# Optimization experiments

Hardware: AMD Instinct MI355X
Metric: run time of the kernel (lower is better)

## Reference

```python
import jax, jax.numpy as jnp
import numpy as np

INPUT_DIM = 8
HIDDEN_DIM = 128
MID = 50
T = 4096
# original: tsteps = linspace(t0, t1, int(2 + (t1-t0)//0.1)); with t1-t0 == 1.0,
# 1.0//0.1 == 9.0 in float arithmetic -> 11 points -> 10 uniform Euler substeps.
K_SUB = 10


def setup_inputs() -> dict:
    key = jax.random.key(0)
    ks = jax.random.split(key, 12)
    x = jax.random.normal(ks[0], (T, INPUT_DIM), dtype=jnp.float32)
    # arange pairs (2i, 2i+1): every interval has t1 - t0 == 1.0
    dt = jnp.arange(T * 2, dtype=jnp.float32).reshape(T, 2)
    s = 0.1  # init.normal_(std=0.1) in LODEFunc; reuse for heads
    W1 = jax.random.normal(ks[1], (INPUT_DIM + HIDDEN_DIM, MID), dtype=jnp.float32) * s
    b1 = jnp.zeros((MID,), dtype=jnp.float32)
    W2 = jax.random.normal(ks[2], (MID, HIDDEN_DIM), dtype=jnp.float32) * s
    b2 = jnp.zeros((HIDDEN_DIM,), dtype=jnp.float32)
    Wls1 = jax.random.normal(ks[3], (HIDDEN_DIM, HIDDEN_DIM), dtype=jnp.float32) * s
    bls1 = jax.random.normal(ks[4], (HIDDEN_DIM,), dtype=jnp.float32) * s
    wls2 = jax.random.normal(ks[5], (HIDDEN_DIM,), dtype=jnp.float32) * s
    bls2 = jax.random.normal(ks[6], (), dtype=jnp.float32) * s
    Wlm1 = jax.random.normal(ks[7], (HIDDEN_DIM, HIDDEN_DIM), dtype=jnp.float32) * s
    blm1 = jax.random.normal(ks[8], (HIDDEN_DIM,), dtype=jnp.float32) * s
    return {"x": x, "dt": dt, "W1": W1, "b1": b1, "W2": W2, "b2": b2,
            "Wls1": Wls1, "bls1": bls1, "wls2": wls2, "bls2": bls2,
            "Wlm1": Wlm1, "blm1": blm1}


def reference(x, dt, W1, b1, W2, b2, Wls1, bls1, wls2, bls2, Wlm1, blm1):
    def ode_func(z, xi):
        # LODEFunc: tanh(Linear(tanh(Linear(cat(z, x)))))
        zx = jnp.concatenate([z, xi])  # [H + I]
        h1 = jnp.tanh(zx @ W1 + b1)    # [50]
        return jnp.tanh(h1 @ W2 + b2)  # [H]

    def step(z, inp):
        xi, dti = inp
        hstep = (dti[1] - dti[0]) / K_SUB  # uniform Euler step (0 interval -> no-op)
        z = jax.lax.fori_loop(0, K_SUB, lambda j, zz: zz + hstep * ode_func(zz, xi), z)
        pre_sigma = jnp.tanh(z @ Wls1 + bls1)
        sigma = jax.nn.softplus(pre_sigma @ wls2 + bls2)
        pre_mu = jnp.tanh(z @ Wlm1 + blm1)
        mu = pre_mu @ wls2 + bls2  # NOTE: original reuses self.ls2 for mu (faithful)
        return z, (mu, sigma)

    z0 = jnp.zeros((HIDDEN_DIM,), dtype=x.dtype)
    _, (mu_out, sigma_out) = jax.lax.scan(step, z0, (x, dt))
    return mu_out[:, None], sigma_out[:, None]  # each [T, 1]
```

## Files before the change

kernel.cpp:

```cpp
#include <hip/hip_runtime.h>
#include <hip/hip_bf16.h>

#define T_STEPS 4096
#define HID 128
#define INP 8
#define MID 50
#define KSUB 10

__device__ __forceinline__ float rlane(float v, int i){
    return __int_as_float(__builtin_amdgcn_readlane(__float_as_int(v), i));
}

__device__ __forceinline__ float fast_tanh(float x){
    float e = __expf(2.0f * x);
    return 1.0f - 2.0f / (e + 1.0f);
}
__device__ __forceinline__ float softplus_f(float x){
    return (x > 20.0f) ? x : __logf(1.0f + __expf(x));
}

__device__ __forceinline__ void wg_barrier(){
    asm volatile("s_waitcnt lgkmcnt(0)\n\ts_barrier" ::: "memory");
}

__global__ __launch_bounds__(384, 2)
void lode_kernel(const float* __restrict__ x, const float* __restrict__ dt,
                 const float* __restrict__ W1, const float* __restrict__ b1,
                 const float* __restrict__ W2, const float* __restrict__ b2,
                 const float* __restrict__ Wls1, const float* __restrict__ bls1,
                 const float* __restrict__ wls2, const float* __restrict__ bls2,
                 const float* __restrict__ Wlm1, const float* __restrict__ blm1,
                 float* __restrict__ out)
{
    __shared__ __align__(16) float pbuf[2][4][64];
    __shared__ __align__(16) float zsnap[2][HID];
    __shared__ __align__(16) float WhL[2][HID*HID];

    const int tid = threadIdx.x;
    const int wid = tid >> 6;
    const int l   = tid & 63;

    {
        float4*       d0 = reinterpret_cast<float4*>(&WhL[0][0]);
        const float4* s0 = reinterpret_cast<const float4*>(Wls1);
        for (int i = tid; i < HID*HID/4; i += 384) d0[i] = s0[i];
        float4*       d1 = reinterpret_cast<float4*>(&WhL[1][0]);
        const float4* s1 = reinterpret_cast<const float4*>(Wlm1);
        for (int i = tid; i < HID*HID/4; i += 384) d1[i] = s1[i];
    }
    wg_barrier();

    if (wid < 4){
        __builtin_amdgcn_s_setprio(1);
        const int base = wid << 5;
        const int lc   = (l < MID) ? l : 0;

        float w1h[32];
        #pragma unroll
        for (int i = 0; i < 32; ++i){
            const float v = W1[(base + i)*MID + lc];
            w1h[i] = (l < MID) ? v : 0.0f;
        }
        float w1x[INP];
        #pragma unroll
        for (int j = 0; j < INP; ++j){
            const float v = W1[(HID + j)*MID + lc];
            w1x[j] = (wid == 0 && l < MID) ? v : 0.0f;
        }
        const float b1c = (wid == 0 && l < MID) ? b1[lc] : 0.0f;

        const int jc = base + (l & 31);
        float w2c[MID];
        #pragma unroll
        for (int k = 0; k < MID; ++k) w2c[k] = W2[k*HID + jc];
        const float b2c = b2[jc];

        float zj = 0.0f;

        float4 xa  = *reinterpret_cast<const float4*>(&x[0]);
        float4 xb  = *reinterpret_cast<const float4*>(&x[4]);
        float2 dtc = *reinterpret_cast<const float2*>(&dt[0]);

        for (int t = 0; t < T_STEPS; ++t){
            const int tn = (t + 1 < T_STEPS) ? t + 1 : t;
            const float4 xan = *reinterpret_cast<const float4*>(&x[tn*INP]);
            const float4 xbn = *reinterpret_cast<const float4*>(&x[tn*INP + 4]);
            const float2 dtn = *reinterpret_cast<const float2*>(&dt[2*tn]);

            float xacc = b1c;
            xacc = fmaf(xa.x, w1x[0], xacc); xacc = fmaf(xa.y, w1x[1], xacc);
            xacc = fmaf(xa.z, w1x[2], xacc); xacc = fmaf(xa.w, w1x[3], xacc);
            xacc = fmaf(xb.x, w1x[4], xacc); xacc = fmaf(xb.y, w1x[5], xacc);
            xacc = fmaf(xb.z, w1x[6], xacc); xacc = fmaf(xb.w, w1x[7], xacc);
            const float hstep = (dtc.y - dtc.x) * (1.0f / KSUB);

            #pragma unroll 2
            for (int s = 0; s < KSUB; ++s){
                float a0 = xacc, a1 = 0.0f, a2 = 0.0f, a3 = 0.0f;
                #pragma unroll
                for (int i = 0; i < 32; i += 4){
                    a0 = fmaf(rlane(zj, i+0), w1h[i+0], a0);
                    a1 = fmaf(rlane(zj, i+1), w1h[i+1], a1);
                    a2 = fmaf(rlane(zj, i+2), w1h[i+2], a2);
                    a3 = fmaf(rlane(zj, i+3), w1h[i+3], a3);
                }
                pbuf[s & 1][wid][l] = (a0 + a1) + (a2 + a3);
                wg_barrier();

                const float p0 = pbuf[s & 1][0][l];
                const float p1 = pbuf[s & 1][1][l];
                const float p2 = pbuf[s & 1][2][l];
                const float p3 = pbuf[s & 1][3][l];
                const float h1v = fast_tanh((p0 + p1) + (p2 + p3));

                float d0 = 0.0f, d1 = 0.0f, d2 = 0.0f, d3 = 0.0f;
                #pragma unroll
                for (int k = 0; k < 48; k += 4){
                    d0 = fmaf(rlane(h1v, k+0), w2c[k+0], d0);
                    d1 = fmaf(rlane(h1v, k+1), w2c[k+1], d1);
                    d2 = fmaf(rlane(h1v, k+2), w2c[k+2], d2);
                    d3 = fmaf(rlane(h1v, k+3), w2c[k+3], d3);
                }
                d0 = fmaf(rlane(h1v, 48), w2c[48], d0);
                d1 = fmaf(rlane(h1v, 49), w2c[49], d1);
                const float d = (d0 + d1) + (d2 + d3);
                zj += hstep * fast_tanh(b2c + d);
            }

            if (l < 32) zsnap[t & 1][base + l] = zj;

            xa = xan; xb = xbn; dtc = dtn;
        }
        wg_barrier();
    } else {
        const float* __restrict__ Wh = (wid == 4) ? &WhL[0][0] : &WhL[1][0];
        const float* __restrict__ bh = (wid == 4) ? bls1 : blm1;
        float2 bhp;   bhp.x = bh[2*l];     bhp.y = bh[2*l+1];
        float2 wls2p; wls2p.x = wls2[2*l]; wls2p.y = wls2[2*l+1];
        const float bls2s = bls2[0];

        for (int t = 0; t <= T_STEPS; ++t){
            if (t < T_STEPS){
                #pragma unroll 2
                for (int s = 0; s < KSUB; ++s) wg_barrier();
            } else {
                wg_barrier();
            }
            if (t == 0) continue;
            const int ts = t - 1;
            const float* zs = &zsnap[ts & 1][0];
            float px = bhp.x, py = bhp.y;
            #pragma unroll 4
            for (int k = 0; k < HID; k += 4){
                const float4 zv = *reinterpret_cast<const float4*>(&zs[k]);
                const float2 a0 = *reinterpret_cast<const float2*>(&Wh[(k+0)*HID + 2*l]);
                const float2 a1 = *reinterpret_cast<const float2*>(&Wh[(k+1)*HID + 2*l]);
                const float2 a2 = *reinterpret_cast<const float2*>(&Wh[(k+2)*HID + 2*l]);
                const float2 a3 = *reinterpret_cast<const float2*>(&Wh[(k+3)*HID + 2*l]);
                px = fmaf(zv.x, a0.x, px); py = fmaf(zv.x, a0.y, py);
                px = fmaf(zv.y, a1.x, px); py = fmaf(zv.y, a1.y, py);
                px = fmaf(zv.z, a2.x, px); py = fmaf(zv.z, a2.y, py);
                px = fmaf(zv.w, a3.x, px); py = fmaf(zv.w, a3.y, py);
            }
            px = fast_tanh(px); py = fast_tanh(py);
            float r = px*wls2p.x + py*wls2p.y;
            #pragma unroll
            for (int off = 1; off < 64; off <<= 1) r += __shfl_xor(r, off, 64);
            if (l == 0){
                if (wid == 4) out[T_STEPS + ts] = softplus_f(r + bls2s);
                else          out[ts]           = r + bls2s;
            }
        }
    }
}

extern "C" void kernel_launch(void* const* d_in, const int* in_sizes, int n_in,
                              void* d_out, int out_size, void* d_ws, size_t ws_size,
                              hipStream_t stream)
{
    const float* x    = (const float*)d_in[0];
    const float* dt   = (const float*)d_in[1];
    const float* W1   = (const float*)d_in[2];
    const float* b1   = (const float*)d_in[3];
    const float* W2   = (const float*)d_in[4];
    const float* b2   = (const float*)d_in[5];
    const float* Wls1 = (const float*)d_in[6];
    const float* bls1 = (const float*)d_in[7];
    const float* wls2 = (const float*)d_in[8];
    const float* bls2 = (const float*)d_in[9];
    const float* Wlm1 = (const float*)d_in[10];
    const float* blm1 = (const float*)d_in[11];
    float* out = (float*)d_out;

    hipLaunchKernelGGL(lode_kernel, dim3(1), dim3(384), 0, stream,
                       x, dt, W1, b1, W2, b2, Wls1, bls1, wls2, bls2, Wlm1, blm1, out);
}
```

Before: 23.05 ms.

## Interleave head-wave matvec across substep barriers and use packed FMA

The two head waves now split their 128x128 matvec for the previous timestep into chunks done between the ten substep barriers, instead of waiting through all barriers and then doing the whole matvec in one go. The reduction and output write are spread over the last two slots, and the final timestep is handled after the loop. The accumulation also switches to a two-wide vector FMA so the compiler can emit packed FP32 FMAs. The aim is to keep the head waves from delaying the barrier-synchronised critical path of the ODE waves, at the cost of more complex control flow.

Result: faster. 18.48 ms, median of 2 (-19.8%).

```diff
diff --git a/kernel.cpp b/kernel.cpp
--- a/kernel.cpp
+++ b/kernel.cpp
@@ -6,6 +6,19 @@
 #define INP 8
 #define MID 50
 #define KSUB 10
+
+typedef float v2f __attribute__((ext_vector_type(2)));
+
+__device__ __forceinline__ v2f mk2(float a, float b){ v2f r; r.x = a; r.y = b; return r; }
+__device__ __forceinline__ v2f bc2(float s){ v2f r; r.x = s; r.y = s; return r; }
+
+__device__ __forceinline__ v2f fma2(v2f a, v2f b, v2f c){
+#if __has_builtin(__builtin_elementwise_fma)
+    return __builtin_elementwise_fma(a, b, c);
+#else
+    c.x = fmaf(a.x, b.x, c.x); c.y = fmaf(a.y, b.y, c.y); return c;
+#endif
+}
 
 __device__ __forceinline__ float rlane(float v, int i){
     return __int_as_float(__builtin_amdgcn_readlane(__float_as_int(v), i));
@@ -135,34 +148,67 @@
     } else {
         const float* __restrict__ Wh = (wid == 4) ? &WhL[0][0] : &WhL[1][0];
         const float* __restrict__ bh = (wid == 4) ? bls1 : blm1;
-        float2 bhp;   bhp.x = bh[2*l];     bhp.y = bh[2*l+1];
-        float2 wls2p; wls2p.x = wls2[2*l]; wls2p.y = wls2[2*l+1];
+        const v2f bhp   = mk2(bh[2*l], bh[2*l+1]);
+        const v2f wls2p = mk2(wls2[2*l], wls2[2*l+1]);
         const float bls2s = bls2[0];
 
-        for (int t = 0; t <= T_STEPS; ++t){
-            if (t < T_STEPS){
-                #pragma unroll 2
-                for (int s = 0; s < KSUB; ++s) wg_barrier();
-            } else {
+        for (int t = 0; t < T_STEPS; ++t){
+            v2f acc2 = bhp;
+            float r = 0.0f;
+            const float* zs = &zsnap[(t - 1) & 1][0];
+            #pragma unroll
+            for (int s = 0; s < KSUB; ++s){
                 wg_barrier();
-            }
-            if (t == 0) continue;
-            const int ts = t - 1;
+                if (t == 0) continue;
+                if (s < 8){
+                    #pragma unroll
+                    for (int kk = 0; kk < 4; ++kk){
+                        const int k = 16*s + 4*kk;
+                        const float4 zv = *reinterpret_cast<const float4*>(&zs[k]);
+                        const v2f w0 = *reinterpret_cast<const v2f*>(&Wh[(k+0)*HID + 2*l]);
+                        const v2f w1 = *reinterpret_cast<const v2f*>(&Wh[(k+1)*HID + 2*l]);
+                        const v2f w2 = *reinterpret_cast<const v2f*>(&Wh[(k+2)*HID + 2*l]);
+                        const v2f w3 = *reinterpret_cast<const v2f*>(&Wh[(k+3)*HID + 2*l]);
+                        acc2 = fma2(bc2(zv.x), w0, acc2);
+                        acc2 = fma2(bc2(zv.y), w1, acc2);
+                        acc2 = fma2(bc2(zv.z), w2, acc2);
+                        acc2 = fma2(bc2(zv.w), w3, acc2);
+                    }
+                } else if (s == 8){
+                    const float px = fast_tanh(acc2.x);
+                    const float py = fast_tanh(acc2.y);
+                    r = px*wls2p.x + py*wls2p.y;
+                    #pragma unroll
+                    for (int off = 1; off < 64; off <<= 1) r += __shfl_xor(r, off, 64);
+                } else {
+                    if (l == 0){
+                        const int ts = t - 1;
+                        if (wid == 4) out[T_STEPS + ts] = softplus_f(r + bls2s);
+                        else          out[ts]           = r + bls2s;
+                    }
+                }
+            }
+        }
+        wg_barrier();
+
+        {
+            const int ts = T_STEPS - 1;
             const float* zs = &zsnap[ts & 1][0];
-            float px = bhp.x, py = bhp.y;
+            v2f acc2 = bhp;
             #pragma unroll 4
             for (int k = 0; k < HID; k += 4){
                 const float4 zv = *reinterpret_cast<const float4*>(&zs[k]);
-                const float2 a0 = *reinterpret_cast<const float2*>(&Wh[(k+0)*HID + 2*l]);
-                const float2 a1 = *reinterpret_cast<const float2*>(&Wh[(k+1)*HID + 2*l]);
-                const float2 a2 = *reinterpret_cast<const float2*>(&Wh[(k+2)*HID + 2*l]);
-                const float2 a3 = *reinterpret_cast<const float2*>(&Wh[(k+3)*HID + 2*l]);
-                px = fmaf(zv.x, a0.x, px); py = fmaf(zv.x, a0.y, py);
-                px = fmaf(zv.y, a1.x, px); py = fmaf(zv.y, a1.y, py);
-                px = fmaf(zv.z, a2.x, px); py = fmaf(zv.z, a2.y, py);
-                px = fmaf(zv.w, a3.x, px); py = fmaf(zv.w, a3.y, py);
-            }
-            px = fast_tanh(px); py = fast_tanh(py);
+                const v2f w0 = *reinterpret_cast<const v2f*>(&Wh[(k+0)*HID + 2*l]);
+                const v2f w1 = *reinterpret_cast<const v2f*>(&Wh[(k+1)*HID + 2*l]);
+                const v2f w2 = *reinterpret_cast<const v2f*>(&Wh[(k+2)*HID + 2*l]);
+                const v2f w3 = *reinterpret_cast<const v2f*>(&Wh[(k+3)*HID + 2*l]);
+                acc2 = fma2(bc2(zv.x), w0, acc2);
+                acc2 = fma2(bc2(zv.y), w1, acc2);
+                acc2 = fma2(bc2(zv.z), w2, acc2);
+                acc2 = fma2(bc2(zv.w), w3, acc2);
+            }
+            const float px = fast_tanh(acc2.x);
+            const float py = fast_tanh(acc2.y);
             float r = px*wls2p.x + py*wls2p.y;
             #pragma unroll
             for (int off = 1; off < 64; off <<= 1) r += __shfl_xor(r, off, 64);
```
